# Optimization experiments

Measured on AMD Instinct MI355X. Metric: run time of the kernel, lower is better.

## Reference

```python
import jax, jax.numpy as jnp
import numpy as np

# DeepSeek-V3-style gate config
TOP_K = 8
N_EXPERTS = 256
N_GROUP = 8
TOPK_GROUP = 4
ROUTED_SCALING = 2.5
EPS = 1e-20


def setup_inputs() -> dict:
    key = jax.random.key(0)
    k1, k2, k3 = jax.random.split(key, 3)
    S, H = 16384, 7168
    hidden_states = jax.random.normal(k1, (S, H), dtype=jnp.float32)
    weight = jax.random.normal(k2, (N_EXPERTS, H), dtype=jnp.float32) * 0.02
    e_score_correction_bias = jax.random.normal(k3, (N_EXPERTS,), dtype=jnp.float32) * 0.1
    return {"hidden_states": hidden_states, "weight": weight,
            "e_score_correction_bias": e_score_correction_bias}


def reference(hidden_states, weight, e_score_correction_bias):
    S = hidden_states.shape[0]
    group_size = N_EXPERTS // N_GROUP  # 32

    # gating GEMM: [S, E]
    router_logits = jnp.einsum('sh,eh->se', hidden_states, weight)
    # scoring_func == 'sigmoid'
    scores = jax.nn.sigmoid(router_logits)
    scores_for_choice = scores + e_score_correction_bias[None, :]

    # group scores: sum of top-2 biased scores within each group -> [S, G]
    grouped = scores_for_choice.reshape(S, N_GROUP, group_size)
    top2_vals, _ = jax.lax.top_k(grouped, 2)
    group_scores = top2_vals.sum(axis=-1)

    # select top `TOPK_GROUP` groups, build group mask
    _, group_idx = jax.lax.top_k(group_scores, TOPK_GROUP)  # [S, topk_group]
    group_mask = jnp.zeros((S, N_GROUP), dtype=scores.dtype)
    group_mask = group_mask.at[jnp.arange(S)[:, None], group_idx].set(1.0)
    score_mask = jnp.repeat(group_mask, group_size, axis=-1)  # [S, E]

    # masked top-k over experts; weights gathered from UNBIASED scores
    tmp_scores = jnp.where(score_mask > 0, scores_for_choice, 0.0)
    _, topk_idx = jax.lax.top_k(tmp_scores, TOP_K)  # [S, top_k]
    topk_weight = jnp.take_along_axis(scores, topk_idx, axis=1)

    # renormalize (top_k > 1 and norm_topk_prob) then scale (noaux_tc)
    denom = topk_weight.sum(axis=-1, keepdims=True) + EPS
    topk_weight = topk_weight / denom * ROUTED_SCALING
    return topk_weight, topk_idx
```

## Files before the change

### kernel.cpp

```cpp
#include <hip/hip_runtime.h>
#include <math.h>

#define H_DIM 7168
#define N_EXP 256
#define N_GRP 8
#define G_SZ  32
#define TOPK_G 4
#define TOPK   8
#define BM 64
#define BK 32
#define S_TOK 16384
#define NTILES (H_DIM / BK)
#define NSPLIT 2
#define NH     (NTILES / NSPLIT)
#define ITILES 4
#define NINT   (NH / ITILES)
#define TILE_W_BYTES 32768

#define SA_SCALE 256.0f
#define SW_SCALE 4096.0f
#define DESCALE  (1.0f / 1048576.0f)

__device__ __align__(256) char g_wimg[(size_t)NTILES * TILE_W_BYTES];
__device__ __align__(256) float g_part[NSPLIT * (size_t)S_TOK * N_EXP];

typedef __attribute__((ext_vector_type(8))) _Float16 f16x8;
typedef __attribute__((ext_vector_type(4))) float f32x4;
typedef __attribute__((ext_vector_type(4))) unsigned short u16x4;
typedef __attribute__((ext_vector_type(8))) unsigned short u16x8;

__device__ inline void split2h(float x, unsigned short& h, unsigned short& l) {
    _Float16 hf = (_Float16)x;
    _Float16 lf = (_Float16)(x - (float)hf);
    h = __builtin_bit_cast(unsigned short, hf);
    l = __builtin_bit_cast(unsigned short, lf);
}

__global__ __launch_bounds__(256)
void convert_w_kernel(const float* __restrict__ W) {
    int idx  = blockIdx.x * 256 + threadIdx.x;
    int e    = idx / (H_DIM / 8);
    int koct = idx - e * (H_DIM / 8);
    int k0   = koct * 8;
    int t    = k0 >> 5;
    int o    = (k0 >> 3) & 3;
    int lane = (e & 15) | (o << 4);
    int w    = e >> 5;
    int nj   = (e >> 4) & 1;
    const float* src = W + (size_t)e * H_DIM + k0;
    unsigned short h[8], l[8];
    #pragma unroll
    for (int j = 0; j < 8; ++j)
        split2h(src[j] * SW_SCALE, h[j], l[j]);
    char* base = g_wimg + (size_t)t * TILE_W_BYTES + (w << 12) + (lane << 4);
    *(u16x8*)(base + nj * 1024)       = u16x8{h[0],h[1],h[2],h[3],h[4],h[5],h[6],h[7]};
    *(u16x8*)(base + (2 + nj) * 1024) = u16x8{l[0],l[1],l[2],l[3],l[4],l[5],l[6],l[7]};
}

__global__ __launch_bounds__(512, 2)
void moe_gemm_half(const float* __restrict__ A)
{
    __shared__ __align__(128) char smem[2 * ITILES * 8192];

    const int tid   = threadIdx.x;
    const int lane  = tid & 63;
    const int wave  = tid >> 6;
    const int b     = blockIdx.x;
    const int khalf = (b >> 2) & 1;
    const int brow  = ((b >> 3) * 4 + (b & 3)) * BM;
    const int g0    = khalf * NH;

    const int fr   = lane & 15;
    const int fkb  = (lane >> 4) << 4;
    const int fswz = ((fr << 6) + fkb) ^ ((fr & 7) << 4);

    const int ar   = tid >> 3;
    const int akq  = tid & 7;
    const int aswz = ((ar << 6) + (akq << 3)) ^ ((ar & 7) << 4);
    const float4* Ag4 = reinterpret_cast<const float4*>(
        A + (size_t)(brow + ar) * H_DIM + khalf * (H_DIM / NSPLIT)) + akq;

    const char* wsrc = g_wimg + (size_t)g0 * TILE_W_BYTES + (wave << 12) + (lane << 4);

    f32x4 acc[4][2] = {};

    auto loadW = [&](int t, f16x8& h0, f16x8& h1, f16x8& l0, f16x8& l1) {
        const char* p = wsrc + (size_t)t * TILE_W_BYTES;
        h0 = *(const f16x8*)(p + 0);
        h1 = *(const f16x8*)(p + 1024);
        l0 = *(const f16x8*)(p + 2048);
        l1 = *(const f16x8*)(p + 3072);
    };

    auto writeA = [&](const float4& v, char* ab) {
        unsigned short h[4], l[4];
        split2h(v.x * SA_SCALE, h[0], l[0]); split2h(v.y * SA_SCALE, h[1], l[1]);
        split2h(v.z * SA_SCALE, h[2], l[2]); split2h(v.w * SA_SCALE, h[3], l[3]);
        *(u16x4*)(ab + aswz)        = u16x4{h[0], h[1], h[2], h[3]};
        *(u16x4*)(ab + 4096 + aswz) = u16x4{l[0], l[1], l[2], l[3]};
    };

    auto compute = [&](const char* ab, f16x8 bh0, f16x8 bh1, f16x8 bl0, f16x8 bl1) {
        f16x8 ah[4], al[4];
        #pragma unroll
        for (int mi = 0; mi < 4; ++mi) {
            ah[mi] = *(const f16x8*)(ab + mi * 1024 + fswz);
            al[mi] = *(const f16x8*)(ab + 4096 + mi * 1024 + fswz);
        }
        __builtin_amdgcn_s_setprio(1);
        #pragma unroll
        for (int mi = 0; mi < 4; ++mi)
            acc[mi][0] = __builtin_amdgcn_mfma_f32_16x16x32_f16(ah[mi], bh0, acc[mi][0], 0, 0, 0);
        #pragma unroll
        for (int mi = 0; mi < 4; ++mi)
            acc[mi][1] = __builtin_amdgcn_mfma_f32_16x16x32_f16(ah[mi], bh1, acc[mi][1], 0, 0, 0);
        #pragma unroll
        for (int mi = 0; mi < 4; ++mi)
            acc[mi][0] = __builtin_amdgcn_mfma_f32_16x16x32_f16(al[mi], bh0, acc[mi][0], 0, 0, 0);
        #pragma unroll
        for (int mi = 0; mi < 4; ++mi)
            acc[mi][1] = __builtin_amdgcn_mfma_f32_16x16x32_f16(al[mi], bh1, acc[mi][1], 0, 0, 0);
        #pragma unroll
        for (int mi = 0; mi < 4; ++mi)
            acc[mi][0] = __builtin_amdgcn_mfma_f32_16x16x32_f16(ah[mi], bl0, acc[mi][0], 0, 0, 0);
        #pragma unroll
        for (int mi = 0; mi < 4; ++mi)
            acc[mi][1] = __builtin_amdgcn_mfma_f32_16x16x32_f16(ah[mi], bl1, acc[mi][1], 0, 0, 0);
        __builtin_amdgcn_s_setprio(0);
    };

    f16x8 xh0, xh1, xl0, xl1;
    f16x8 yh0, yh1, yl0, yl1;

    {
        char* b0 = smem;
        float4 a0[ITILES];
        #pragma unroll
        for (int s = 0; s < ITILES; ++s) a0[s] = Ag4[(size_t)s * 8];
        loadW(0, xh0, xh1, xl0, xl1);
        loadW(1, yh0, yh1, yl0, yl1);
        #pragma unroll
        for (int s = 0; s < ITILES; ++s) writeA(a0[s], b0 + s * 8192);
        asm volatile("s_waitcnt lgkmcnt(0)" ::: "memory");
        __builtin_amdgcn_s_barrier();
    }

    #pragma unroll 1
    for (int i = 0; i < NINT; ++i) {
        char* cur = smem + (i & 1) * (ITILES * 8192);
        char* nxt = smem + ((i + 1) & 1) * (ITILES * 8192);
        const bool havenext = (i + 1 < NINT);
        const int ibase = (havenext ? i + 1 : i) * ITILES;

        float4 an[ITILES];
        #pragma unroll
        for (int s = 0; s < ITILES; ++s) an[s] = Ag4[(size_t)(ibase + s) * 8];

        #pragma unroll
        for (int s = 0; s < ITILES; ++s) {
            const int t = i * ITILES + s;
            const int tpf = (t + 2 < NH) ? t + 2 : NH - 1;
            f16x8 nh0, nh1, nl0, nl1;
            loadW(tpf, nh0, nh1, nl0, nl1);
            compute(cur + s * 8192, xh0, xh1, xl0, xl1);
            if (s == 1 && havenext) {
                #pragma unroll
                for (int ss = 0; ss < ITILES; ++ss)
                    writeA(an[ss], nxt + ss * 8192);
            }
            xh0 = yh0; xh1 = yh1; xl0 = yl0; xl1 = yl1;
            yh0 = nh0; yh1 = nh1; yl0 = nl0; yl1 = nl1;
        }
        asm volatile("s_waitcnt lgkmcnt(0)" ::: "memory");
        __builtin_amdgcn_s_barrier();
    }

    float* pb = g_part + ((size_t)khalf * S_TOK + brow) * N_EXP;
    #pragma unroll
    for (int mi = 0; mi < 4; ++mi)
        #pragma unroll
        for (int nj = 0; nj < 2; ++nj)
            #pragma unroll
            for (int q = 0; q < 4; ++q) {
                int row = mi * 16 + ((lane >> 4) << 2) + q;
                int col = wave * 32 + nj * 16 + (lane & 15);
                pb[row * N_EXP + col] = acc[mi][nj][q];
            }
}

__global__ __launch_bounds__(256)
void gate_kernel(const float* __restrict__ bias, float* __restrict__ out, int S)
{
    const int lane = threadIdx.x & 63;
    const int row  = (blockIdx.x * 256 + threadIdx.x) >> 6;

    const float4 p0 = *(const float4*)(g_part + (size_t)row * N_EXP + lane * 4);
    const float4 p1 = *(const float4*)(g_part + ((size_t)S_TOK + row) * N_EXP + lane * 4);
    const float4 b4 = *(const float4*)(bias + lane * 4);

    float s[4], v[4];
    float m1 = -1e30f, m2 = -1e30f;
    {
        const float* q0 = (const float*)&p0;
        const float* q1 = (const float*)&p1;
        const float* qb = (const float*)&b4;
        #pragma unroll
        for (int j = 0; j < 4; ++j) {
            float x = (q0[j] + q1[j]) * DESCALE;
            s[j] = 1.0f / (1.0f + expf(-x));
            float sb = s[j] + qb[j];
            v[j] = sb;
            if (sb > m1) { m2 = m1; m1 = sb; } else if (sb > m2) { m2 = sb; }
        }
    }
    #pragma unroll
    for (int d = 1; d < 8; d <<= 1) {
        float om1 = __shfl_xor(m1, d), om2 = __shfl_xor(m2, d);
        float hi = fmaxf(m1, om1), lo = fminf(m1, om1);
        m1 = hi;
        m2 = fmaxf(lo, fmaxf(m2, om2));
    }
    float gs = m1 + m2;
    float gsv[8];
    #pragma unroll
    for (int g = 0; g < 8; ++g) gsv[g] = __shfl(gs, g << 3);

    unsigned gmask = 0;
    #pragma unroll
    for (int t = 0; t < TOPK_G; ++t) {
        float best = -1e30f; int bg = 0;
        #pragma unroll
        for (int g = 0; g < 8; ++g) {
            bool avail = !((gmask >> g) & 1);
            if (avail && gsv[g] > best) { best = gsv[g]; bg = g; }
        }
        gmask |= 1u << bg;
    }

    const bool sel = (gmask >> (lane >> 3)) & 1;
    #pragma unroll
    for (int j = 0; j < 4; ++j) v[j] = sel ? v[j] : 0.0f;

    float wv[TOPK]; int wi[TOPK]; float wsum = 0.0f;
    #pragma unroll
    for (int t = 0; t < TOPK; ++t) {
        float bv = v[0]; int bj = 0;
        #pragma unroll
        for (int j = 1; j < 4; ++j)
            if (v[j] > bv) { bv = v[j]; bj = j; }
        int bidx = (lane << 2) | bj;
        #pragma unroll
        for (int d = 32; d >= 1; d >>= 1) {
            float ov = __shfl_xor(bv, d);
            int   oi = __shfl_xor(bidx, d);
            if (ov > bv || (ov == bv && oi < bidx)) { bv = ov; bidx = oi; }
        }
        int ol = bidx >> 2, oj = bidx & 3;
        float sl = s[0];
        if (oj == 1) sl = s[1]; else if (oj == 2) sl = s[2]; else if (oj == 3) sl = s[3];
        float sv = __shfl(sl, ol);
        wv[t] = sv; wi[t] = bidx; wsum += sv;
        if (lane == ol) {
            if (oj == 0) v[0] = -1e30f; else if (oj == 1) v[1] = -1e30f;
            else if (oj == 2) v[2] = -1e30f; else v[3] = -1e30f;
        }
    }

    if (lane == 0) {
        float scale = 2.5f / (wsum + 1e-20f);
        #pragma unroll
        for (int t = 0; t < TOPK; ++t) {
            out[(size_t)row * TOPK + t] = wv[t] * scale;
            out[(size_t)S * TOPK + (size_t)row * TOPK + t] = (float)wi[t];
        }
    }
}

extern "C" void kernel_launch(void* const* d_in, const int* in_sizes, int n_in,
                              void* d_out, int out_size, void* d_ws, size_t ws_size,
                              hipStream_t stream) {
    const float* A    = (const float*)d_in[0];
    const float* W    = (const float*)d_in[1];
    const float* bias = (const float*)d_in[2];
    float* out = (float*)d_out;
    const int S = in_sizes[0] / H_DIM;

    convert_w_kernel<<<dim3(N_EXP * (H_DIM / 8) / 256), 256, 0, stream>>>(W);
    moe_gemm_half<<<dim3(NSPLIT * S / BM), 512, 0, stream>>>(A);
    gate_kernel<<<dim3(S / 4), 256, 0, stream>>>(bias, out, S);
}
```

Baseline: 217.7 us.

## Re-tile GEMM waves as 2x4 grid over rows and experts, reduce W prefetch depth

Changes the per-wave output tile from 64 rows x 32 experts to 32 rows x 64 experts (waves arranged 2 along M, 4 along N), with the weight image layout reorganized to match. Each wave now reads half the A fragments from LDS per tile but twice as many weight fragments from global memory, and weight prefetch is reduced from two tiles ahead to one, with low-half weights loaded just in time. The aim is to cut LDS read traffic and register pressure, at the cost of doubled global/L2 weight traffic per wave and less latency hiding for weight loads.

```diff
diff --git a/kernel.cpp b/kernel.cpp
--- a/kernel.cpp
+++ b/kernel.cpp
@@ -45,16 +45,16 @@
     int t    = k0 >> 5;
     int o    = (k0 >> 3) & 3;
     int lane = (e & 15) | (o << 4);
-    int w    = e >> 5;
-    int nj   = (e >> 4) & 1;
+    int eq   = e >> 6;
+    int nj   = (e >> 4) & 3;
     const float* src = W + (size_t)e * H_DIM + k0;
     unsigned short h[8], l[8];
     #pragma unroll
     for (int j = 0; j < 8; ++j)
         split2h(src[j] * SW_SCALE, h[j], l[j]);
-    char* base = g_wimg + (size_t)t * TILE_W_BYTES + (w << 12) + (lane << 4);
-    *(u16x8*)(base + nj * 1024)       = u16x8{h[0],h[1],h[2],h[3],h[4],h[5],h[6],h[7]};
-    *(u16x8*)(base + (2 + nj) * 1024) = u16x8{l[0],l[1],l[2],l[3],l[4],l[5],l[6],l[7]};
+    char* base = g_wimg + (size_t)t * TILE_W_BYTES + (eq << 13) + (nj << 10) + (lane << 4);
+    *(u16x8*)(base)        = u16x8{h[0],h[1],h[2],h[3],h[4],h[5],h[6],h[7]};
+    *(u16x8*)(base + 4096) = u16x8{l[0],l[1],l[2],l[3],l[4],l[5],l[6],l[7]};
 }
 
 __global__ __launch_bounds__(512, 2)
@@ -65,14 +65,16 @@
     const int tid   = threadIdx.x;
     const int lane  = tid & 63;
     const int wave  = tid >> 6;
+    const int mh    = wave >> 2;
+    const int eq    = wave & 3;
     const int b     = blockIdx.x;
     const int khalf = (b >> 2) & 1;
     const int brow  = ((b >> 3) * 4 + (b & 3)) * BM;
-    const int g0    = khalf * NH;
 
     const int fr   = lane & 15;
     const int fkb  = (lane >> 4) << 4;
     const int fswz = ((fr << 6) + fkb) ^ ((fr & 7) << 4);
+    const int abase = (mh << 11) + fswz;
 
     const int ar   = tid >> 3;
     const int akq  = tid & 7;
@@ -80,18 +82,27 @@
     const float4* Ag4 = reinterpret_cast<const float4*>(
         A + (size_t)(brow + ar) * H_DIM + khalf * (H_DIM / NSPLIT)) + akq;
 
-    const char* wsrc = g_wimg + (size_t)g0 * TILE_W_BYTES + (wave << 12) + (lane << 4);
-
-    f32x4 acc[4][2] = {};
-
-    auto loadW = [&](int t, f16x8& h0, f16x8& h1, f16x8& l0, f16x8& l1) {
+    const char* wsrc = g_wimg + (size_t)(khalf * NH) * TILE_W_BYTES
+                       + (eq << 13) + (lane << 4);
+
+    f32x4 acc[2][4] = {};
+    f16x8 whiX[4], whiY[4], wlo[4];
+
+    auto loadWhiX = [&](int t) {
         const char* p = wsrc + (size_t)t * TILE_W_BYTES;
-        h0 = *(const f16x8*)(p + 0);
-        h1 = *(const f16x8*)(p + 1024);
-        l0 = *(const f16x8*)(p + 2048);
-        l1 = *(const f16x8*)(p + 3072);
-    };
-
+        #pragma unroll
+        for (int nj = 0; nj < 4; ++nj) whiX[nj] = *(const f16x8*)(p + (nj << 10));
+    };
+    auto loadWhiY = [&](int t) {
+        const char* p = wsrc + (size_t)t * TILE_W_BYTES;
+        #pragma unroll
+        for (int nj = 0; nj < 4; ++nj) whiY[nj] = *(const f16x8*)(p + (nj << 10));
+    };
+    auto loadWlo = [&](int t) {
+        const char* p = wsrc + (size_t)t * TILE_W_BYTES + 4096;
+        #pragma unroll
+        for (int nj = 0; nj < 4; ++nj) wlo[nj] = *(const f16x8*)(p + (nj << 10));
+    };
     auto writeA = [&](const float4& v, char* ab) {
         unsigned short h[4], l[4];
         split2h(v.x * SA_SCALE, h[0], l[0]); split2h(v.y * SA_SCALE, h[1], l[1]);
@@ -99,46 +110,39 @@
         *(u16x4*)(ab + aswz)        = u16x4{h[0], h[1], h[2], h[3]};
         *(u16x4*)(ab + 4096 + aswz) = u16x4{l[0], l[1], l[2], l[3]};
     };
-
-    auto compute = [&](const char* ab, f16x8 bh0, f16x8 bh1, f16x8 bl0, f16x8 bl1) {
-        f16x8 ah[4], al[4];
-        #pragma unroll
-        for (int mi = 0; mi < 4; ++mi) {
-            ah[mi] = *(const f16x8*)(ab + mi * 1024 + fswz);
-            al[mi] = *(const f16x8*)(ab + 4096 + mi * 1024 + fswz);
-        }
+    auto tileMFMA = [&](const char* ab, const f16x8* whi) {
+        f16x8 ah0 = *(const f16x8*)(ab + abase);
+        f16x8 ah1 = *(const f16x8*)(ab + abase + 1024);
+        f16x8 al0 = *(const f16x8*)(ab + 4096 + abase);
+        f16x8 al1 = *(const f16x8*)(ab + 4096 + abase + 1024);
         __builtin_amdgcn_s_setprio(1);
         #pragma unroll
-        for (int mi = 0; mi < 4; ++mi)
-            acc[mi][0] = __builtin_amdgcn_mfma_f32_16x16x32_f16(ah[mi], bh0, acc[mi][0], 0, 0, 0);
-        #pragma unroll
-        for (int mi = 0; mi < 4; ++mi)
-            acc[mi][1] = __builtin_amdgcn_mfma_f32_16x16x32_f16(ah[mi], bh1, acc[mi][1], 0, 0, 0);
-        #pragma unroll
-        for (int mi = 0; mi < 4; ++mi)
-            acc[mi][0] = __builtin_amdgcn_mfma_f32_16x16x32_f16(al[mi], bh0, acc[mi][0], 0, 0, 0);
-        #pragma unroll
-        for (int mi = 0; mi < 4; ++mi)
-            acc[mi][1] = __builtin_amdgcn_mfma_f32_16x16x32_f16(al[mi], bh1, acc[mi][1], 0, 0, 0);
-        #pragma unroll
-        for (int mi = 0; mi < 4; ++mi)
-            acc[mi][0] = __builtin_amdgcn_mfma_f32_16x16x32_f16(ah[mi], bl0, acc[mi][0], 0, 0, 0);
-        #pragma unroll
-        for (int mi = 0; mi < 4; ++mi)
-            acc[mi][1] = __builtin_amdgcn_mfma_f32_16x16x32_f16(ah[mi], bl1, acc[mi][1], 0, 0, 0);
+        for (int nj = 0; nj < 4; ++nj)
+            acc[0][nj] = __builtin_amdgcn_mfma_f32_16x16x32_f16(ah0, whi[nj], acc[0][nj], 0, 0, 0);
+        #pragma unroll
+        for (int nj = 0; nj < 4; ++nj)
+            acc[1][nj] = __builtin_amdgcn_mfma_f32_16x16x32_f16(ah1, whi[nj], acc[1][nj], 0, 0, 0);
+        #pragma unroll
+        for (int nj = 0; nj < 4; ++nj)
+            acc[0][nj] = __builtin_amdgcn_mfma_f32_16x16x32_f16(al0, whi[nj], acc[0][nj], 0, 0, 0);
+        #pragma unroll
+        for (int nj = 0; nj < 4; ++nj)
+            acc[1][nj] = __builtin_amdgcn_mfma_f32_16x16x32_f16(al1, whi[nj], acc[1][nj], 0, 0, 0);
+        #pragma unroll
+        for (int nj = 0; nj < 4; ++nj)
+            acc[0][nj] = __builtin_amdgcn_mfma_f32_16x16x32_f16(ah0, wlo[nj], acc[0][nj], 0, 0, 0);
+        #pragma unroll
+        for (int nj = 0; nj < 4; ++nj)
+            acc[1][nj] = __builtin_amdgcn_mfma_f32_16x16x32_f16(ah1, wlo[nj], acc[1][nj], 0, 0, 0);
         __builtin_amdgcn_s_setprio(0);
     };
-
-    f16x8 xh0, xh1, xl0, xl1;
-    f16x8 yh0, yh1, yl0, yl1;
 
     {
         char* b0 = smem;
         float4 a0[ITILES];
         #pragma unroll
         for (int s = 0; s < ITILES; ++s) a0[s] = Ag4[(size_t)s * 8];
-        loadW(0, xh0, xh1, xl0, xl1);
-        loadW(1, yh0, yh1, yl0, yl1);
+        loadWhiX(0);
         #pragma unroll
         for (int s = 0; s < ITILES; ++s) writeA(a0[s], b0 + s * 8192);
         asm volatile("s_waitcnt lgkmcnt(0)" ::: "memory");
@@ -159,17 +163,15 @@
         #pragma unroll
         for (int s = 0; s < ITILES; ++s) {
             const int t = i * ITILES + s;
-            const int tpf = (t + 2 < NH) ? t + 2 : NH - 1;
-            f16x8 nh0, nh1, nl0, nl1;
-            loadW(tpf, nh0, nh1, nl0, nl1);
-            compute(cur + s * 8192, xh0, xh1, xl0, xl1);
+            const int tpf = (t + 1 < NH) ? t + 1 : NH - 1;
+            loadWlo(t);
+            if (s & 1) loadWhiX(tpf); else loadWhiY(tpf);
+            tileMFMA(cur + s * 8192, (s & 1) ? whiY : whiX);
             if (s == 1 && havenext) {
                 #pragma unroll
                 for (int ss = 0; ss < ITILES; ++ss)
                     writeA(an[ss], nxt + ss * 8192);
             }
-            xh0 = yh0; xh1 = yh1; xl0 = yl0; xl1 = yl1;
-            yh0 = nh0; yh1 = nh1; yl0 = nl0; yl1 = nl1;
         }
         asm volatile("s_waitcnt lgkmcnt(0)" ::: "memory");
         __builtin_amdgcn_s_barrier();
@@ -177,13 +179,13 @@
 
     float* pb = g_part + ((size_t)khalf * S_TOK + brow) * N_EXP;
     #pragma unroll
-    for (int mi = 0; mi < 4; ++mi)
-        #pragma unroll
-        for (int nj = 0; nj < 2; ++nj)
+    for (int mi = 0; mi < 2; ++mi)
+        #pragma unroll
+        for (int nj = 0; nj < 4; ++nj)
             #pragma unroll
             for (int q = 0; q < 4; ++q) {
-                int row = mi * 16 + ((lane >> 4) << 2) + q;
-                int col = wave * 32 + nj * 16 + (lane & 15);
+                int row = (mh << 5) + (mi << 4) + ((lane >> 4) << 2) + q;
+                int col = (eq << 6) + (nj << 4) + (lane & 15);
                 pb[row * N_EXP + col] = acc[mi][nj][q];
             }
 }
```

New measurement: 251.6 us. 1.16x slower.

## Fuse split-K GEMM and gating into one 1024-thread block per row tile

Applied to the files above, without the earlier changes.

Each 64-row tile now runs in one 1024-thread block in which two groups of 8 waves handle the two K halves. The partial sums are reduced through shared memory, and the sigmoid plus grouped top-k gating run in the same kernel. This removes the global partial-sum buffer (two S×256 float arrays written and read back) and one kernel launch. In exchange it uses about 128KB of LDS per block at occupancy 1, and the two K halves no longer run as independent blocks, which may reduce latency hiding.

```diff
diff --git a/kernel.cpp b/kernel.cpp
--- a/kernel.cpp
+++ b/kernel.cpp
@@ -11,8 +11,7 @@
 #define BK 32
 #define S_TOK 16384
 #define NTILES (H_DIM / BK)
-#define NSPLIT 2
-#define NH     (NTILES / NSPLIT)
+#define NH     (NTILES / 2)
 #define ITILES 4
 #define NINT   (NH / ITILES)
 #define TILE_W_BYTES 32768
@@ -21,8 +20,9 @@
 #define SW_SCALE 4096.0f
 #define DESCALE  (1.0f / 1048576.0f)
 
+#define SMEM_BYTES 131328
+
 __device__ __align__(256) char g_wimg[(size_t)NTILES * TILE_W_BYTES];
-__device__ __align__(256) float g_part[NSPLIT * (size_t)S_TOK * N_EXP];
 
 typedef __attribute__((ext_vector_type(8))) _Float16 f16x8;
 typedef __attribute__((ext_vector_type(4))) float f32x4;
@@ -57,30 +57,33 @@
     *(u16x8*)(base + (2 + nj) * 1024) = u16x8{l[0],l[1],l[2],l[3],l[4],l[5],l[6],l[7]};
 }
 
-__global__ __launch_bounds__(512, 2)
-void moe_gemm_half(const float* __restrict__ A)
+__global__ __launch_bounds__(1024, 1)
+void moe_fused(const float* __restrict__ A, const float* __restrict__ bias,
+               float* __restrict__ out, int S)
 {
-    __shared__ __align__(128) char smem[2 * ITILES * 8192];
-
-    const int tid   = threadIdx.x;
-    const int lane  = tid & 63;
-    const int wave  = tid >> 6;
-    const int b     = blockIdx.x;
-    const int khalf = (b >> 2) & 1;
-    const int brow  = ((b >> 3) * 4 + (b & 3)) * BM;
-    const int g0    = khalf * NH;
+    __shared__ __align__(128) char smem[SMEM_BYTES];
+
+    const int tid  = threadIdx.x;
+    const int lane = tid & 63;
+    const int wave = tid >> 6;
+    const int kseg = wave >> 3;
+    const int wq   = wave & 7;
+    const int brow = blockIdx.x * BM;
 
     const int fr   = lane & 15;
     const int fkb  = (lane >> 4) << 4;
     const int fswz = ((fr << 6) + fkb) ^ ((fr & 7) << 4);
 
-    const int ar   = tid >> 3;
-    const int akq  = tid & 7;
+    const int ts   = tid & 511;
+    const int ar   = ts >> 3;
+    const int akq  = ts & 7;
     const int aswz = ((ar << 6) + (akq << 3)) ^ ((ar & 7) << 4);
     const float4* Ag4 = reinterpret_cast<const float4*>(
-        A + (size_t)(brow + ar) * H_DIM + khalf * (H_DIM / NSPLIT)) + akq;
-
-    const char* wsrc = g_wimg + (size_t)g0 * TILE_W_BYTES + (wave << 12) + (lane << 4);
+        A + (size_t)(brow + ar) * H_DIM + kseg * (H_DIM / 2)) + akq;
+
+    const char* wsrc = g_wimg + (size_t)(kseg * NH) * TILE_W_BYTES
+                       + (wq << 12) + (lane << 4);
+    char* const aregion = smem + kseg * 65536;
 
     f32x4 acc[4][2] = {};
 
@@ -133,22 +136,21 @@
     f16x8 yh0, yh1, yl0, yl1;
 
     {
-        char* b0 = smem;
         float4 a0[ITILES];
         #pragma unroll
         for (int s = 0; s < ITILES; ++s) a0[s] = Ag4[(size_t)s * 8];
         loadW(0, xh0, xh1, xl0, xl1);
         loadW(1, yh0, yh1, yl0, yl1);
         #pragma unroll
-        for (int s = 0; s < ITILES; ++s) writeA(a0[s], b0 + s * 8192);
+        for (int s = 0; s < ITILES; ++s) writeA(a0[s], aregion + s * 8192);
         asm volatile("s_waitcnt lgkmcnt(0)" ::: "memory");
         __builtin_amdgcn_s_barrier();
     }
 
     #pragma unroll 1
     for (int i = 0; i < NINT; ++i) {
-        char* cur = smem + (i & 1) * (ITILES * 8192);
-        char* nxt = smem + ((i + 1) & 1) * (ITILES * 8192);
+        char* cur = aregion + (i & 1) * 32768;
+        char* nxt = aregion + ((i + 1) & 1) * 32768;
         const bool havenext = (i + 1 < NINT);
         const int ibase = (havenext ? i + 1 : i) * ITILES;
 
@@ -175,103 +177,115 @@
         __builtin_amdgcn_s_barrier();
     }
 
-    float* pb = g_part + ((size_t)khalf * S_TOK + brow) * N_EXP;
-    #pragma unroll
-    for (int mi = 0; mi < 4; ++mi)
-        #pragma unroll
-        for (int nj = 0; nj < 2; ++nj)
-            #pragma unroll
-            for (int q = 0; q < 4; ++q) {
-                int row = mi * 16 + ((lane >> 4) << 2) + q;
-                int col = wave * 32 + nj * 16 + (lane & 15);
-                pb[row * N_EXP + col] = acc[mi][nj][q];
-            }
-}
-
-__global__ __launch_bounds__(256)
-void gate_kernel(const float* __restrict__ bias, float* __restrict__ out, int S)
-{
-    const int lane = threadIdx.x & 63;
-    const int row  = (blockIdx.x * 256 + threadIdx.x) >> 6;
-
-    const float4 p0 = *(const float4*)(g_part + (size_t)row * N_EXP + lane * 4);
-    const float4 p1 = *(const float4*)(g_part + ((size_t)S_TOK + row) * N_EXP + lane * 4);
+    float* Ps = (float*)smem;
+    float* Sc = (float*)(smem + 65536);
+    if (kseg == 0) {
+        #pragma unroll
+        for (int mi = 0; mi < 4; ++mi)
+            #pragma unroll
+            for (int nj = 0; nj < 2; ++nj)
+                #pragma unroll
+                for (int q = 0; q < 4; ++q) {
+                    int row = mi * 16 + ((lane >> 4) << 2) + q;
+                    int col = (wq << 5) + (nj << 4) + (lane & 15);
+                    Ps[row * 256 + col] = acc[mi][nj][q];
+                }
+    }
+    __syncthreads();
+    if (kseg == 1) {
+        #pragma unroll
+        for (int mi = 0; mi < 4; ++mi)
+            #pragma unroll
+            for (int nj = 0; nj < 2; ++nj)
+                #pragma unroll
+                for (int q = 0; q < 4; ++q) {
+                    int row = mi * 16 + ((lane >> 4) << 2) + q;
+                    int col = (wq << 5) + (nj << 4) + (lane & 15);
+                    float x = (Ps[row * 256 + col] + acc[mi][nj][q]) * DESCALE;
+                    Sc[row * 257 + col] = 1.0f / (1.0f + expf(-x));
+                }
+    }
+    __syncthreads();
+
     const float4 b4 = *(const float4*)(bias + lane * 4);
-
-    float s[4], v[4];
-    float m1 = -1e30f, m2 = -1e30f;
-    {
-        const float* q0 = (const float*)&p0;
-        const float* q1 = (const float*)&p1;
-        const float* qb = (const float*)&b4;
-        #pragma unroll
-        for (int j = 0; j < 4; ++j) {
-            float x = (q0[j] + q1[j]) * DESCALE;
-            s[j] = 1.0f / (1.0f + expf(-x));
-            float sb = s[j] + qb[j];
-            v[j] = sb;
-            if (sb > m1) { m2 = m1; m1 = sb; } else if (sb > m2) { m2 = sb; }
-        }
-    }
-    #pragma unroll
-    for (int d = 1; d < 8; d <<= 1) {
-        float om1 = __shfl_xor(m1, d), om2 = __shfl_xor(m2, d);
-        float hi = fmaxf(m1, om1), lo = fminf(m1, om1);
-        m1 = hi;
-        m2 = fmaxf(lo, fmaxf(m2, om2));
-    }
-    float gs = m1 + m2;
-    float gsv[8];
-    #pragma unroll
-    for (int g = 0; g < 8; ++g) gsv[g] = __shfl(gs, g << 3);
-
-    unsigned gmask = 0;
-    #pragma unroll
-    for (int t = 0; t < TOPK_G; ++t) {
-        float best = -1e30f; int bg = 0;
-        #pragma unroll
-        for (int g = 0; g < 8; ++g) {
-            bool avail = !((gmask >> g) & 1);
-            if (avail && gsv[g] > best) { best = gsv[g]; bg = g; }
-        }
-        gmask |= 1u << bg;
-    }
-
-    const bool sel = (gmask >> (lane >> 3)) & 1;
-    #pragma unroll
-    for (int j = 0; j < 4; ++j) v[j] = sel ? v[j] : 0.0f;
-
-    float wv[TOPK]; int wi[TOPK]; float wsum = 0.0f;
-    #pragma unroll
-    for (int t = 0; t < TOPK; ++t) {
-        float bv = v[0]; int bj = 0;
-        #pragma unroll
-        for (int j = 1; j < 4; ++j)
-            if (v[j] > bv) { bv = v[j]; bj = j; }
-        int bidx = (lane << 2) | bj;
-        #pragma unroll
-        for (int d = 32; d >= 1; d >>= 1) {
-            float ov = __shfl_xor(bv, d);
-            int   oi = __shfl_xor(bidx, d);
-            if (ov > bv || (ov == bv && oi < bidx)) { bv = ov; bidx = oi; }
-        }
-        int ol = bidx >> 2, oj = bidx & 3;
-        float sl = s[0];
-        if (oj == 1) sl = s[1]; else if (oj == 2) sl = s[2]; else if (oj == 3) sl = s[3];
-        float sv = __shfl(sl, ol);
-        wv[t] = sv; wi[t] = bidx; wsum += sv;
-        if (lane == ol) {
-            if (oj == 0) v[0] = -1e30f; else if (oj == 1) v[1] = -1e30f;
-            else if (oj == 2) v[2] = -1e30f; else v[3] = -1e30f;
-        }
-    }
-
-    if (lane == 0) {
-        float scale = 2.5f / (wsum + 1e-20f);
+    #pragma unroll 1
+    for (int rr = 0; rr < 4; ++rr) {
+        const int lrow = (wave << 2) + rr;
+        const int row  = brow + lrow;
+        const float* srow = Sc + lrow * 257;
+
+        float s[4], v[4];
+        float m1 = -1e30f, m2 = -1e30f;
+        {
+            const float* qb = (const float*)&b4;
+            #pragma unroll
+            for (int j = 0; j < 4; ++j) {
+                s[j] = srow[lane * 4 + j];
+                float sb = s[j] + qb[j];
+                v[j] = sb;
+                if (sb > m1) { m2 = m1; m1 = sb; } else if (sb > m2) { m2 = sb; }
+            }
+        }
+        #pragma unroll
+        for (int d = 1; d < 8; d <<= 1) {
+            float om1 = __shfl_xor(m1, d), om2 = __shfl_xor(m2, d);
+            float hi = fmaxf(m1, om1), lo = fminf(m1, om1);
+            m1 = hi;
+            m2 = fmaxf(lo, fmaxf(m2, om2));
+        }
+        float gs = m1 + m2;
+        float gsv[8];
+        #pragma unroll
+        for (int g = 0; g < 8; ++g) gsv[g] = __shfl(gs, g << 3);
+
+        unsigned gmask = 0;
+        #pragma unroll
+        for (int t = 0; t < TOPK_G; ++t) {
+            float best = -1e30f; int bg = 0;
+            #pragma unroll
+            for (int g = 0; g < 8; ++g) {
+                bool avail = !((gmask >> g) & 1);
+                if (avail && gsv[g] > best) { best = gsv[g]; bg = g; }
+            }
+            gmask |= 1u << bg;
+        }
+
+        const bool sel = (gmask >> (lane >> 3)) & 1;
+        #pragma unroll
+        for (int j = 0; j < 4; ++j) v[j] = sel ? v[j] : 0.0f;
+
+        float wv[TOPK]; int wi[TOPK]; float wsum = 0.0f;
         #pragma unroll
         for (int t = 0; t < TOPK; ++t) {
-            out[(size_t)row * TOPK + t] = wv[t] * scale;
-            out[(size_t)S * TOPK + (size_t)row * TOPK + t] = (float)wi[t];
+            float bv = v[0]; int bj = 0;
+            #pragma unroll
+            for (int j = 1; j < 4; ++j)
+                if (v[j] > bv) { bv = v[j]; bj = j; }
+            int bidx = (lane << 2) | bj;
+            #pragma unroll
+            for (int d = 32; d >= 1; d >>= 1) {
+                float ov = __shfl_xor(bv, d);
+                int   oi = __shfl_xor(bidx, d);
+                if (ov > bv || (ov == bv && oi < bidx)) { bv = ov; bidx = oi; }
+            }
+            int ol = bidx >> 2, oj = bidx & 3;
+            float sl = s[0];
+            if (oj == 1) sl = s[1]; else if (oj == 2) sl = s[2]; else if (oj == 3) sl = s[3];
+            float sv = __shfl(sl, ol);
+            wv[t] = sv; wi[t] = bidx; wsum += sv;
+            if (lane == ol) {
+                if (oj == 0) v[0] = -1e30f; else if (oj == 1) v[1] = -1e30f;
+                else if (oj == 2) v[2] = -1e30f; else v[3] = -1e30f;
+            }
+        }
+
+        if (lane == 0) {
+            float scale = 2.5f / (wsum + 1e-20f);
+            #pragma unroll
+            for (int t = 0; t < TOPK; ++t) {
+                out[(size_t)row * TOPK + t] = wv[t] * scale;
+                out[(size_t)S * TOPK + (size_t)row * TOPK + t] = (float)wi[t];
+            }
         }
     }
 }
@@ -286,6 +300,5 @@
     const int S = in_sizes[0] / H_DIM;
 
     convert_w_kernel<<<dim3(N_EXP * (H_DIM / 8) / 256), 256, 0, stream>>>(W);
-    moe_gemm_half<<<dim3(NSPLIT * S / BM), 512, 0, stream>>>(A);
-    gate_kernel<<<dim3(S / 4), 256, 0, stream>>>(bias, out, S);
+    moe_fused<<<dim3(S / BM), 1024, 0, stream>>>(A, bias, out, S);
 }
```

Result: no change. 218.6 us (+0.4%).

## Drop W register prefetch pipeline and halve LDS stage to raise occupancy

Applied to the files above, without the earlier changes.

Removes the two-tile-ahead register prefetch of the weight fragments, so each tile now loads its W fragments right before its MFMAs. It also halves the A tiles per LDS stage from 4 to 2 and raises the launch-bounds minimum blocks per CU from 2 to 6. Fewer live registers and less LDS let more waves share each CU and hide load latency through occupancy rather than software pipelining. The risk is exposed global-load latency per tile and more barriers per K step, and register pressure at the higher bound may force spills.

```diff
diff --git a/kernel.cpp b/kernel.cpp
--- a/kernel.cpp
+++ b/kernel.cpp
@@ -13,7 +13,7 @@
 #define NTILES (H_DIM / BK)
 #define NSPLIT 2
 #define NH     (NTILES / NSPLIT)
-#define ITILES 4
+#define ITILES 2
 #define NINT   (NH / ITILES)
 #define TILE_W_BYTES 32768
 
@@ -57,7 +57,7 @@
     *(u16x8*)(base + (2 + nj) * 1024) = u16x8{l[0],l[1],l[2],l[3],l[4],l[5],l[6],l[7]};
 }
 
-__global__ __launch_bounds__(512, 2)
+__global__ __launch_bounds__(512, 6)
 void moe_gemm_half(const float* __restrict__ A)
 {
     __shared__ __align__(128) char smem[2 * ITILES * 8192];
@@ -68,7 +68,6 @@
     const int b     = blockIdx.x;
     const int khalf = (b >> 2) & 1;
     const int brow  = ((b >> 3) * 4 + (b & 3)) * BM;
-    const int g0    = khalf * NH;
 
     const int fr   = lane & 15;
     const int fkb  = (lane >> 4) << 4;
@@ -80,17 +79,10 @@
     const float4* Ag4 = reinterpret_cast<const float4*>(
         A + (size_t)(brow + ar) * H_DIM + khalf * (H_DIM / NSPLIT)) + akq;
 
-    const char* wsrc = g_wimg + (size_t)g0 * TILE_W_BYTES + (wave << 12) + (lane << 4);
+    const char* wsrc = g_wimg + (size_t)(khalf * NH) * TILE_W_BYTES
+                       + (wave << 12) + (lane << 4);
 
     f32x4 acc[4][2] = {};
-
-    auto loadW = [&](int t, f16x8& h0, f16x8& h1, f16x8& l0, f16x8& l1) {
-        const char* p = wsrc + (size_t)t * TILE_W_BYTES;
-        h0 = *(const f16x8*)(p + 0);
-        h1 = *(const f16x8*)(p + 1024);
-        l0 = *(const f16x8*)(p + 2048);
-        l1 = *(const f16x8*)(p + 3072);
-    };
 
     auto writeA = [&](const float4& v, char* ab) {
         unsigned short h[4], l[4];
@@ -100,7 +92,12 @@
         *(u16x4*)(ab + 4096 + aswz) = u16x4{l[0], l[1], l[2], l[3]};
     };
 
-    auto compute = [&](const char* ab, f16x8 bh0, f16x8 bh1, f16x8 bl0, f16x8 bl1) {
+    auto doTile = [&](int t, const char* ab) {
+        const char* p = wsrc + (size_t)t * TILE_W_BYTES;
+        f16x8 bh0 = *(const f16x8*)(p + 0);
+        f16x8 bh1 = *(const f16x8*)(p + 1024);
+        f16x8 bl0 = *(const f16x8*)(p + 2048);
+        f16x8 bl1 = *(const f16x8*)(p + 3072);
         f16x8 ah[4], al[4];
         #pragma unroll
         for (int mi = 0; mi < 4; ++mi) {
@@ -129,18 +126,12 @@
         __builtin_amdgcn_s_setprio(0);
     };
 
-    f16x8 xh0, xh1, xl0, xl1;
-    f16x8 yh0, yh1, yl0, yl1;
-
     {
-        char* b0 = smem;
         float4 a0[ITILES];
         #pragma unroll
         for (int s = 0; s < ITILES; ++s) a0[s] = Ag4[(size_t)s * 8];
-        loadW(0, xh0, xh1, xl0, xl1);
-        loadW(1, yh0, yh1, yl0, yl1);
-        #pragma unroll
-        for (int s = 0; s < ITILES; ++s) writeA(a0[s], b0 + s * 8192);
+        #pragma unroll
+        for (int s = 0; s < ITILES; ++s) writeA(a0[s], smem + s * 8192);
         asm volatile("s_waitcnt lgkmcnt(0)" ::: "memory");
         __builtin_amdgcn_s_barrier();
     }
@@ -158,18 +149,12 @@
 
         #pragma unroll
         for (int s = 0; s < ITILES; ++s) {
-            const int t = i * ITILES + s;
-            const int tpf = (t + 2 < NH) ? t + 2 : NH - 1;
-            f16x8 nh0, nh1, nl0, nl1;
-            loadW(tpf, nh0, nh1, nl0, nl1);
-            compute(cur + s * 8192, xh0, xh1, xl0, xl1);
+            doTile(i * ITILES + s, cur + s * 8192);
             if (s == 1 && havenext) {
                 #pragma unroll
                 for (int ss = 0; ss < ITILES; ++ss)
                     writeA(an[ss], nxt + ss * 8192);
             }
-            xh0 = yh0; xh1 = yh1; xl0 = yl0; xl1 = yl1;
-            yh0 = nh0; yh1 = nh1; yl0 = nl0; yl1 = nl1;
         }
         asm volatile("s_waitcnt lgkmcnt(0)" ::: "memory");
         __builtin_amdgcn_s_barrier();
@@ -183,7 +168,7 @@
             #pragma unroll
             for (int q = 0; q < 4; ++q) {
                 int row = mi * 16 + ((lane >> 4) << 2) + q;
-                int col = wave * 32 + nj * 16 + (lane & 15);
+                int col = (wave << 5) + (nj << 4) + (lane & 15);
                 pb[row * N_EXP + col] = acc[mi][nj][q];
             }
 }
```

New measurement: 433.0 us. 1.99x slower.
